# Performance work log

Measured on AMD Instinct MI355X. Metric: run time of the kernel, lower is better.

## Reference

```python
import jax, jax.numpy as jnp
import numpy as np

B, S, F, D, H, L = 32, 512, 40, 512, 8, 4
T = S + 1
DK, DV = D // 2, D          # expand_k=0.5, expand_v=1.0 (fla GLA defaults)
HK, HV = DK // H, DV // H
GLR = 16                    # gate low-rank dim
GLN = 16.0                  # gate logit normalizer
MLP = 4 * D


def sin_pos(t, d, n=10000.0):
    pos = jnp.arange(t, dtype=jnp.float32)[:, None]
    den = jnp.power(n, 2.0 * jnp.arange(d // 2, dtype=jnp.float32) / d)
    e = jnp.zeros((t, d), jnp.float32)
    e = e.at[:, 0::2].set(jnp.sin(pos / den))
    e = e.at[:, 1::2].set(jnp.cos(pos / den))
    return e


def layernorm(x, w, b, eps=1e-5):
    m = x.mean(-1, keepdims=True)
    v = ((x - m) ** 2).mean(-1, keepdims=True)
    return (x - m) * jax.lax.rsqrt(v + eps) * w + b


def bin_norm(x, l1, b1, l2, b2, y1, y2):
    # x: (b, f, s). BiN: temporal z-norm with per-feature affine (X2) +
    # feature z-norm with per-time affine (X1); unbiased std, small std -> 1.
    st = jnp.sqrt(x.var(axis=2, ddof=1, keepdims=True))
    st = jnp.where(st < 1e-4, 1.0, st)
    Z2 = (x - x.mean(axis=2, keepdims=True)) / st
    X2 = l2[None, :, None] * Z2 + b2[None, :, None]
    sf = jnp.sqrt(x.var(axis=1, ddof=1, keepdims=True))
    sf = jnp.where(sf < 1e-4, 1.0, sf)
    Z1 = (x - x.mean(axis=1, keepdims=True)) / sf
    X1 = l1[None, None, :] * Z1 + b1[None, None, :]
    return y1 * X1 + y2 * X2


def gla_attn(x, qw, kw, vw, gw, gkw1, gkw2, gkb2, gnw, ow):
    # Gated linear attention, recurrent form: S_t = exp(gk_t) * S_{t-1} + k_t v_t^T
    b, t, _ = x.shape
    q = (x @ qw).reshape(b, t, H, HK) * (HK ** -0.5)
    k = (x @ kw).reshape(b, t, H, HK)
    v = (x @ vw).reshape(b, t, H, HV)
    g = (x @ gw).reshape(b, t, H, HV)
    gk = (jax.nn.log_sigmoid((x @ gkw1) @ gkw2 + gkb2) / GLN).reshape(b, t, H, HK)

    def step(Sc, inp):
        qt, kt, vt, gt = inp                       # (b,H,HK),(b,H,HK),(b,H,HV),(b,H,HK)
        Sc = Sc * jnp.exp(gt)[..., None] + kt[..., None] * vt[..., None, :]
        return Sc, jnp.einsum('bhk,bhkv->bhv', qt, Sc)

    init = jnp.zeros((b, H, HK, HV), x.dtype)
    to_t = lambda a: jnp.swapaxes(a, 0, 1)        # (t, b, H, dim)
    _, o = jax.lax.scan(step, init, (to_t(q), to_t(k), to_t(v), to_t(gk)))
    o = jnp.swapaxes(o, 0, 1)                     # (b, t, H, HV)
    o = o * jax.lax.rsqrt((o * o).mean(-1, keepdims=True) + 1e-5) * gnw  # head RMSNorm
    o = o * g * jax.nn.sigmoid(g)                 # swish output gate
    return o.reshape(b, t, DV) @ ow


def setup_inputs():
    key = jax.random.key(0)
    ks = iter(jax.random.split(key, 64))
    r = lambda shape, s=0.02: jax.random.normal(next(ks), shape, jnp.float32) * s
    return dict(
        x=jax.random.normal(next(ks), (B, S, F), jnp.float32),
        bin_l1=r((S,), 0.1), bin_b1=jnp.zeros((S,), jnp.float32),
        bin_l2=r((F,), 0.1), bin_b2=jnp.zeros((F,), jnp.float32),
        bin_y1=jnp.float32(0.5), bin_y2=jnp.float32(0.5),
        emb_w=r((F, D)), emb_b=jnp.zeros((D,), jnp.float32),
        cls_token=jnp.zeros((D,), jnp.float32),
        ln1_w=jnp.ones((L, D), jnp.float32), ln1_b=jnp.zeros((L, D), jnp.float32),
        q_w=r((L, D, DK)), k_w=r((L, D, DK)), v_w=r((L, D, DV)), g_w=r((L, D, DV)),
        gk_w1=r((L, D, GLR)), gk_w2=r((L, GLR, DK)), gk_b2=jnp.zeros((L, DK), jnp.float32),
        gnorm_w=jnp.ones((L, HV), jnp.float32),
        o_w=r((L, DV, D)),
        ln2_w=jnp.ones((L, D), jnp.float32), ln2_b=jnp.zeros((L, D), jnp.float32),
        mlp_w1=r((L, D, MLP)), mlp_b1=jnp.zeros((L, MLP), jnp.float32),
        mlp_w2=r((L, MLP, D)), mlp_b2=jnp.zeros((L, D), jnp.float32),
        head_w=r((D, 3)), head_b=jnp.zeros((3,), jnp.float32),
    )


def reference(x, bin_l1, bin_b1, bin_l2, bin_b2, bin_y1, bin_y2, emb_w, emb_b,
              cls_token, ln1_w, ln1_b, q_w, k_w, v_w, g_w, gk_w1, gk_w2, gk_b2,
              gnorm_w, o_w, ln2_w, ln2_b, mlp_w1, mlp_b1, mlp_w2, mlp_b2,
              head_w, head_b):
    h = bin_norm(jnp.swapaxes(x, 1, 2), bin_l1, bin_b1, bin_l2, bin_b2, bin_y1, bin_y2)
    h = jnp.swapaxes(h, 1, 2) @ emb_w + emb_b                    # (b, s, D)
    cls = jnp.broadcast_to(cls_token, (h.shape[0], 1, D))
    h = jnp.concatenate([h, cls], axis=1) + sin_pos(T, D)[None]  # (b, s+1, D)
    for i in range(L):
        a = gla_attn(layernorm(h, ln1_w[i], ln1_b[i]), q_w[i], k_w[i], v_w[i],
                     g_w[i], gk_w1[i], gk_w2[i], gk_b2[i], gnorm_w[i], o_w[i])
        h = h + a
        m = layernorm(h, ln2_w[i], ln2_b[i])
        m = jax.nn.gelu(m @ mlp_w1[i] + mlp_b1[i], approximate=False)
        h = h + m @ mlp_w2[i] + mlp_b2[i]
    return h[:, -1] @ head_w + head_b                            # (b, 3)
```

## Files before the change

### kernel.cpp

```cpp
#include <hip/hip_runtime.h>
#include <hip/hip_bf16.h>
#include <hip/hip_fp16.h>
#include <math.h>

#define Bsz   32
#define Ssz   512
#define Fsz   40
#define Dsz   512
#define Hh    8
#define Lnum  4
#define Tsz   513
#define DKsz  256
#define DVsz  512
#define HKsz  32
#define HVsz  64
#define Msz   (Bsz*Tsz)
#define Mpad  16512
#define MLPsz 2048
#define NCH   16
#define CSZ   33
#define QKVG  1536
#define VOFF  8404992

typedef __attribute__((ext_vector_type(4))) float f32x4;
typedef __attribute__((ext_vector_type(8))) short bf16x8;

__device__ __forceinline__ float bf2f(short s) {
  unsigned int u = ((unsigned int)(unsigned short)s) << 16;
  return __builtin_bit_cast(float, u);
}
__device__ __forceinline__ short f2bf(float f) {
  __hip_bfloat16 b = __float2bfloat16(f);
  return __builtin_bit_cast(short, b);
}

__device__ __forceinline__ float wave_sum(float v) {
#pragma unroll
  for (int off = 32; off > 0; off >>= 1) v += __shfl_xor(v, off, 64);
  return v;
}

__global__ void pos_kernel(float* __restrict__ pos) {
  int idx = blockIdx.x * 256 + threadIdx.x;
  if (idx >= Tsz * Dsz) return;
  int t = idx / Dsz, d = idx % Dsz;
  float e = (float)(2 * (d >> 1)) / (float)Dsz;
  float den = powf(10000.f, e);
  float a = (float)t / den;
  pos[idx] = (d & 1) ? cosf(a) : sinf(a);
}

__global__ void tstat_kernel(const float* __restrict__ x,
                             float* __restrict__ mt, float* __restrict__ rst) {
  int bf = blockIdx.x;
  int b = bf / Fsz, f = bf % Fsz;
  int lane = threadIdx.x;
  const float* xp = x + (size_t)b * Ssz * Fsz + f;
  float s = 0.f, sq = 0.f;
  for (int i = lane; i < Ssz; i += 64) {
    float v = xp[(size_t)i * Fsz];
    s += v; sq += v * v;
  }
  s = wave_sum(s); sq = wave_sum(sq);
  if (lane == 0) {
    float m = s / (float)Ssz;
    float var = (sq - (float)Ssz * m * m) / (float)(Ssz - 1);
    float st = sqrtf(fmaxf(var, 0.f));
    if (st < 1e-4f) st = 1.f;
    mt[bf] = m;
    rst[bf] = 1.f / st;
  }
}

__global__ __launch_bounds__(64) void binorm_kernel(
    const float* __restrict__ x, const float* __restrict__ l1,
    const float* __restrict__ b1, const float* __restrict__ l2,
    const float* __restrict__ b2, const float* __restrict__ y1p,
    const float* __restrict__ y2p, const float* __restrict__ mt,
    const float* __restrict__ rst, float* __restrict__ xbT) {
  int row = blockIdx.x;
  int lane = threadIdx.x;
  int b = row / Tsz, t = row % Tsz;
  bool valid = (row < Msz) && (t < Ssz);
  if (!valid) {
    if (lane < Fsz) xbT[(size_t)lane * Mpad + row] = 0.f;
    return;
  }
  float xv = 0.f;
  const float* xp = x + ((size_t)b * Ssz + t) * Fsz;
  if (lane < Fsz) xv = xp[lane];
  float s  = wave_sum(lane < Fsz ? xv : 0.f);
  float sq = wave_sum(lane < Fsz ? xv * xv : 0.f);
  float m = s / (float)Fsz;
  float var = (sq - (float)Fsz * m * m) / (float)(Fsz - 1);
  float sf = sqrtf(fmaxf(var, 0.f));
  if (sf < 1e-4f) sf = 1.f;
  if (lane < Fsz) {
    float y1 = y1p[0], y2 = y2p[0];
    float z1 = (xv - m) / sf;
    float X1 = l1[t] * z1 + b1[t];
    int bf = b * Fsz + lane;
    float z2 = (xv - mt[bf]) * rst[bf];
    float X2 = l2[lane] * z2 + b2[lane];
    xbT[(size_t)lane * Mpad + row] = y1 * X1 + y2 * X2;
  }
}

__global__ __launch_bounds__(256, 4) void embgemm_kernel(
    const float* __restrict__ xbT, const float* __restrict__ emb_w,
    const float* __restrict__ emb_b, const float* __restrict__ cls,
    const float* __restrict__ pos, float* __restrict__ h) {
  __shared__ float as[Fsz][64];
  __shared__ float bs[Fsz][64];
  int tid = threadIdx.x, tx = tid & 15, ty = tid >> 4;
  int r0 = blockIdx.x * 64, c0 = blockIdx.y * 64;
  for (int idx = tid; idx < Fsz * 64; idx += 256) {
    int f = idx >> 6, r = idx & 63;
    as[f][r] = xbT[(size_t)f * Mpad + r0 + r];
    bs[f][r] = emb_w[f * Dsz + c0 + r];
  }
  __syncthreads();
  float acc[4][4] = {};
#pragma unroll 5
  for (int f = 0; f < Fsz; ++f) {
    float4 a = *(const float4*)&as[f][ty * 4];
    float4 bv = *(const float4*)&bs[f][tx * 4];
    float av[4] = {a.x, a.y, a.z, a.w};
    float bw[4] = {bv.x, bv.y, bv.z, bv.w};
#pragma unroll
    for (int i = 0; i < 4; ++i)
#pragma unroll
      for (int j = 0; j < 4; ++j) acc[i][j] += av[i] * bw[j];
  }
#pragma unroll
  for (int i = 0; i < 4; ++i) {
    int gm = r0 + ty * 4 + i;
    int t = gm % Tsz;
    const float* pp = pos + (size_t)t * Dsz;
    bool iscls = (t == Ssz);
    int gn = c0 + tx * 4;
#pragma unroll
    for (int j = 0; j < 4; ++j) {
      float v = iscls ? (cls[gn + j] + pp[gn + j])
                      : (acc[i][j] + emb_b[gn + j] + pp[gn + j]);
      h[(size_t)gm * Dsz + gn + j] = v;
    }
  }
}

__global__ __launch_bounds__(64) void ln_kernel(
    const float* __restrict__ in, const float* __restrict__ w,
    const float* __restrict__ b, short* __restrict__ out) {
  int row = blockIdx.x, lane = threadIdx.x;
  const float* p = in + (size_t)row * Dsz;
  float4 v0 = *(const float4*)(p + lane * 8);
  float4 v1 = *(const float4*)(p + lane * 8 + 4);
  float s  = v0.x + v0.y + v0.z + v0.w + v1.x + v1.y + v1.z + v1.w;
  float sq = v0.x*v0.x + v0.y*v0.y + v0.z*v0.z + v0.w*v0.w
           + v1.x*v1.x + v1.y*v1.y + v1.z*v1.z + v1.w*v1.w;
  s = wave_sum(s); sq = wave_sum(sq);
  float m = s * (1.f / Dsz);
  float var = sq * (1.f / Dsz) - m * m;
  float r = rsqrtf(var + 1e-5f);
  float4 w0 = *(const float4*)(w + lane * 8);
  float4 w1 = *(const float4*)(w + lane * 8 + 4);
  float4 b0 = *(const float4*)(b + lane * 8);
  float4 b1v = *(const float4*)(b + lane * 8 + 4);
  bf16x8 pk;
  pk[0] = f2bf((v0.x - m) * r * w0.x + b0.x);
  pk[1] = f2bf((v0.y - m) * r * w0.y + b0.y);
  pk[2] = f2bf((v0.z - m) * r * w0.z + b0.z);
  pk[3] = f2bf((v0.w - m) * r * w0.w + b0.w);
  pk[4] = f2bf((v1.x - m) * r * w1.x + b1v.x);
  pk[5] = f2bf((v1.y - m) * r * w1.y + b1v.y);
  pk[6] = f2bf((v1.z - m) * r * w1.z + b1v.z);
  pk[7] = f2bf((v1.w - m) * r * w1.w + b1v.w);
  *(bf16x8*)(out + (size_t)row * Dsz + lane * 8) = pk;
}

__global__ __launch_bounds__(256) void wtall_kernel(
    const float* __restrict__ qw, const float* __restrict__ kw,
    const float* __restrict__ vw, const float* __restrict__ gw,
    const float* __restrict__ ow, const float* __restrict__ m1w,
    const float* __restrict__ m2w, short* __restrict__ qkvT,
    short* __restrict__ owT, short* __restrict__ m1T, short* __restrict__ m2T) {
  __shared__ float t[32][33];
  int bid = blockIdx.x;
  int tx = threadIdx.x & 31, ty = threadIdx.x >> 5;
  const float* W; short* Wt; int K, N, k0, n0, nD;
  if (bid < 768) {
    int kx = bid & 15, ny = bid >> 4;
    int n0g = ny * 32;
    int ld;
    if (n0g < 256)       { W = qw; n0 = n0g;        ld = DKsz; }
    else if (n0g < 512)  { W = kw; n0 = n0g - 256;  ld = DKsz; }
    else if (n0g < 1024) { W = vw; n0 = n0g - 512;  ld = DVsz; }
    else                 { W = gw; n0 = n0g - 1024; ld = DVsz; }
    k0 = kx * 32; K = Dsz; N = ld; Wt = qkvT; nD = n0g;
  } else if (bid < 1024) {
    int idx = bid - 768;
    k0 = (idx & 15) * 32; n0 = (idx >> 4) * 32;
    W = ow; Wt = owT; K = DVsz; N = Dsz; nD = n0;
  } else if (bid < 2048) {
    int idx = bid - 1024;
    k0 = (idx & 15) * 32; n0 = (idx >> 4) * 32;
    W = m1w; Wt = m1T; K = Dsz; N = MLPsz; nD = n0;
  } else {
    int idx = bid - 2048;
    k0 = (idx & 63) * 32; n0 = (idx >> 6) * 32;
    W = m2w; Wt = m2T; K = MLPsz; N = Dsz; nD = n0;
  }
#pragma unroll
  for (int r = 0; r < 32; r += 8)
    t[ty + r][tx] = W[(size_t)(k0 + ty + r) * N + n0 + tx];
  __syncthreads();
#pragma unroll
  for (int r = 0; r < 32; r += 8)
    Wt[(size_t)(nD + ty + r) * K + k0 + tx] = f2bf(t[tx][ty + r]);
}

template<int ACT, int OBF, int SCAT>
__global__ __launch_bounds__(256) void mgemm_kernel(
    const short* __restrict__ A, const short* __restrict__ Bt,
    void* __restrict__ Cv, const float* __restrict__ bias,
    const float* __restrict__ resid, int N, int K) {
  __shared__ short As[128 * 64];
  __shared__ short Bs[128 * 64];
  int tid = threadIdx.x;
  int lane = tid & 63, wid = tid >> 6;
  int wr = wid >> 1, wc = wid & 1;
  int m0 = blockIdx.x * 128, n0 = blockIdx.y * 128;
  f32x4 acc[4][4];
#pragma unroll
  for (int i = 0; i < 4; ++i)
#pragma unroll
    for (int j = 0; j < 4; ++j) acc[i][j] = (f32x4){0.f, 0.f, 0.f, 0.f};

  int kq = lane >> 4;
  int rsel = lane & 15;

  for (int kt = 0; kt < K; kt += 64) {
#pragma unroll
    for (int i = 0; i < 4; ++i) {
      int li = i * 256 + tid;
      int row = li >> 3;
      int gsrc = (li & 7) ^ (row & 7);
      const short* ga = A + (size_t)(m0 + row) * K + kt + gsrc * 8;
      const short* gb = Bt + (size_t)(n0 + row) * K + kt + gsrc * 8;
      int base = (i * 256 + wid * 64) * 8;
      __builtin_amdgcn_global_load_lds(
          (const __attribute__((address_space(1))) unsigned int*)ga,
          (__attribute__((address_space(3))) unsigned int*)&As[base], 16, 0, 0);
      __builtin_amdgcn_global_load_lds(
          (const __attribute__((address_space(1))) unsigned int*)gb,
          (__attribute__((address_space(3))) unsigned int*)&Bs[base], 16, 0, 0);
    }
    __syncthreads();
#pragma unroll
    for (int s = 0; s < 2; ++s) {
      bf16x8 af[4], bfr[4];
#pragma unroll
      for (int i = 0; i < 4; ++i) {
        int row = wr * 64 + i * 16 + rsel;
        int slot = (s * 4 + kq) ^ (row & 7);
        af[i] = *(const bf16x8*)&As[row * 64 + slot * 8];
        int col = wc * 64 + i * 16 + rsel;
        int slotB = (s * 4 + kq) ^ (col & 7);
        bfr[i] = *(const bf16x8*)&Bs[col * 64 + slotB * 8];
      }
#pragma unroll
      for (int i = 0; i < 4; ++i)
#pragma unroll
        for (int j = 0; j < 4; ++j)
          acc[i][j] = __builtin_amdgcn_mfma_f32_16x16x32_bf16(af[i], bfr[j], acc[i][j], 0, 0, 0);
    }
    __syncthreads();
  }

#pragma unroll
  for (int i = 0; i < 4; ++i) {
    int rbase = m0 + wr * 64 + i * 16 + (lane >> 4) * 4;
#pragma unroll
    for (int j = 0; j < 4; ++j) {
      int gn = n0 + wc * 64 + j * 16 + (lane & 15);
      float bv = (SCAT == 0 && bias) ? bias[gn] : 0.f;
#pragma unroll
      for (int r = 0; r < 4; ++r) {
        int gm = rbase + r;
        float v = acc[i][j][r] + bv;
        if (SCAT == 0) {
          if (ACT == 1) v = 0.5f * v * (1.f + erff(v * 0.70710678118654752f));
          if (resid) v += resid[(size_t)gm * N + gn];
          if (OBF) ((short*)Cv)[(size_t)gm * N + gn] = f2bf(v);
          else     ((float*)Cv)[(size_t)gm * N + gn] = v;
        } else {
          if (gm < Msz) {
            int bq = gm / Tsz, tq = gm - bq * Tsz;
            if (gn < 512) {
              int hq = (gn >> 5) & 7;
              int off = (gn & 31) | ((gn & 256) >> 3);
              ((float*)Cv)[(((size_t)bq * 8 + hq) * Tsz + tq) * 64 + off] = v;
            } else if (gn < 1024) {
              int hq = (gn >> 6) & 7;
              ((float*)Cv)[(size_t)VOFF + (((size_t)bq * 8 + hq) * Tsz + tq) * 64 + (gn & 63)] = v;
            } else {
              int hq = (gn >> 6) & 7;
              ((__half*)const_cast<float*>(resid))[(((size_t)bq * 8 + hq) * Tsz + tq) * 64 + (gn & 63)] = __float2half(v);
            }
          }
        }
      }
    }
  }
}

__global__ __launch_bounds__(64) void gk12_kernel(const short* __restrict__ xn,
    const float* __restrict__ w1, const float* __restrict__ w2,
    const float* __restrict__ b2, float* __restrict__ gkeP) {
  int m = blockIdx.x, lane = threadIdx.x;
  __shared__ float xr[512];
  __shared__ float y[16];
  bf16x8 v = *(const bf16x8*)(xn + (size_t)m * Dsz + lane * 8);
#pragma unroll
  for (int e = 0; e < 8; ++e) xr[lane * 8 + e] = bf2f(v[e]);
  __syncthreads();
  int c = lane & 15, q = lane >> 4;
  float acc = 0.f;
#pragma unroll 8
  for (int i = 0; i < 128; ++i) {
    int k = q * 128 + i;
    acc += xr[k] * w1[k * 16 + c];
  }
  acc += __shfl_xor(acc, 16, 64);
  acc += __shfl_xor(acc, 32, 64);
  if (lane < 16) y[c] = acc;
  __syncthreads();
  int b = m / Tsz, t = m - b * Tsz;
#pragma unroll
  for (int p = 0; p < 4; ++p) {
    int n = lane + p * 64;
    float z = b2[n];
#pragma unroll
    for (int r = 0; r < 16; ++r) z += y[r] * w2[r * 256 + n];
    float ls = (z >= 0.f) ? -log1pf(expf(-z)) : z - log1pf(expf(z));
    int hq = n >> 5;
    gkeP[(((size_t)b * 8 + hq) * Tsz + t) * 32 + (n & 31)] = expf(ls * 0.0625f);
  }
}

__global__ __launch_bounds__(64) void scanA_kernel(
    const float* __restrict__ qkP, const float* __restrict__ gkeP,
    float* __restrict__ Ac, float* __restrict__ Bc) {
  int gid = blockIdx.x;
  int bh = gid >> 4, c = gid & 15;
  int lane = threadIdx.x;
  int t0 = c * CSZ;
  int nst = min(CSZ, Tsz - t0);
  __shared__ __align__(16) float s_k[CSZ * 32];
  __shared__ __align__(16) float s_g[CSZ * 32];
  __shared__ __align__(16) float s_v[CSZ * 64];
  const size_t rowbase = (size_t)bh * Tsz + t0;
  const float* qksrc = qkP + rowbase * 64;
  const float* vsrc  = qkP + (size_t)VOFF + rowbase * 64;
  const float* gsrc  = gkeP + rowbase * 32;
  int nkg = nst * 8;
#pragma unroll
  for (int i = 0; i < 5; ++i) {
    int gi = i * 64 + lane;
    if (gi < nkg) {
      int st = gi >> 3, g4 = (gi & 7) * 4;
      __builtin_amdgcn_global_load_lds(
        (const __attribute__((address_space(1))) unsigned int*)(qksrc + (size_t)st * 64 + 32 + g4),
        (__attribute__((address_space(3))) unsigned int*)s_k + i * 256, 16, 0, 0);
      __builtin_amdgcn_global_load_lds(
        (const __attribute__((address_space(1))) unsigned int*)(gsrc + (size_t)gi * 4),
        (__attribute__((address_space(3))) unsigned int*)s_g + i * 256, 16, 0, 0);
    }
  }
  int nv = nst * 16;
#pragma unroll
  for (int i = 0; i < 9; ++i) {
    int gi = i * 64 + lane;
    if (gi < nv)
      __builtin_amdgcn_global_load_lds(
        (const __attribute__((address_space(1))) unsigned int*)(vsrc + (size_t)gi * 4),
        (__attribute__((address_space(3))) unsigned int*)s_v + i * 256, 16, 0, 0);
  }
  float S[32];
#pragma unroll
  for (int i = 0; i < 32; ++i) S[i] = 0.f;
  float ac = 1.f;
  __syncthreads();
  for (int ts = 0; ts < nst; ++ts) {
    float vv = s_v[ts * 64 + lane];
#pragma unroll
    for (int j = 0; j < 8; ++j) {
      float4 kk = *(const float4*)&s_k[ts * 32 + j * 4];
      float4 gg = *(const float4*)&s_g[ts * 32 + j * 4];
      S[4*j+0] = S[4*j+0] * gg.x + kk.x * vv;
      S[4*j+1] = S[4*j+1] * gg.y + kk.y * vv;
      S[4*j+2] = S[4*j+2] * gg.z + kk.z * vv;
      S[4*j+3] = S[4*j+3] * gg.w + kk.w * vv;
    }
    ac *= s_g[ts * 32 + (lane & 31)];
  }
  float* bp = Bc + ((size_t)gid * 64 + lane) * 32;
#pragma unroll
  for (int j = 0; j < 8; ++j)
    *(float4*)(bp + j * 4) = make_float4(S[4*j+0], S[4*j+1], S[4*j+2], S[4*j+3]);
  if (lane < 32) Ac[(size_t)gid * 32 + lane] = ac;
}

__global__ __launch_bounds__(64) void scanB_kernel(
    const float* __restrict__ Ac, float* __restrict__ Bc) {
  int bh = blockIdx.x;
  int lane = threadIdx.x;
  float cur[32];
#pragma unroll
  for (int i = 0; i < 32; ++i) cur[i] = 0.f;
  __shared__ float sA[32];
  for (int c = 0; c < NCH; ++c) {
    size_t gid = (size_t)bh * NCH + c;
    float* bp = Bc + (gid * 64 + lane) * 32;
    __syncthreads();
    if (lane < 32) sA[lane] = Ac[gid * 32 + lane];
    __syncthreads();
    float4 tb[8];
#pragma unroll
    for (int j = 0; j < 8; ++j) tb[j] = *(const float4*)(bp + j * 4);
#pragma unroll
    for (int j = 0; j < 8; ++j)
      *(float4*)(bp + j * 4) = make_float4(cur[4*j+0], cur[4*j+1], cur[4*j+2], cur[4*j+3]);
#pragma unroll
    for (int j = 0; j < 8; ++j) {
      cur[4*j+0] = sA[4*j+0] * cur[4*j+0] + tb[j].x;
      cur[4*j+1] = sA[4*j+1] * cur[4*j+1] + tb[j].y;
      cur[4*j+2] = sA[4*j+2] * cur[4*j+2] + tb[j].z;
      cur[4*j+3] = sA[4*j+3] * cur[4*j+3] + tb[j].w;
    }
  }
}

__global__ __launch_bounds__(64) void scanC_kernel(
    const float* __restrict__ qkP, const __half* __restrict__ gP,
    const float* __restrict__ gkeP, const float* __restrict__ gnw,
    const float* __restrict__ Bc, short* __restrict__ att) {
  int gid = blockIdx.x;
  int bh = gid >> 4, c = gid & 15;
  int b = bh >> 3, hh = bh & 7;
  int lane = threadIdx.x;
  int t0 = c * CSZ;
  int nst = min(CSZ, Tsz - t0);
  __shared__ __align__(16) float s_qk[CSZ * 64];
  __shared__ __align__(16) float s_g[CSZ * 32];
  __shared__ __align__(16) float s_v[CSZ * 64];
  __shared__ __align__(16) __half s_gt[CSZ * 64];
  const size_t rowbase = (size_t)bh * Tsz + t0;
  const float* qksrc = qkP + rowbase * 64;
  const float* vsrc  = qkP + (size_t)VOFF + rowbase * 64;
  const float* gsrc  = gkeP + rowbase * 32;
  const __half* gtsrc = gP + rowbase * 64;
  int n16 = nst * 16;
#pragma unroll
  for (int i = 0; i < 9; ++i) {
    int gi = i * 64 + lane;
    if (gi < n16) {
      __builtin_amdgcn_global_load_lds(
        (const __attribute__((address_space(1))) unsigned int*)(qksrc + (size_t)gi * 4),
        (__attribute__((address_space(3))) unsigned int*)s_qk + i * 256, 16, 0, 0);
      __builtin_amdgcn_global_load_lds(
        (const __attribute__((address_space(1))) unsigned int*)(vsrc + (size_t)gi * 4),
        (__attribute__((address_space(3))) unsigned int*)s_v + i * 256, 16, 0, 0);
    }
  }
  int n8 = nst * 8;
#pragma unroll
  for (int i = 0; i < 5; ++i) {
    int gi = i * 64 + lane;
    if (gi < n8) {
      __builtin_amdgcn_global_load_lds(
        (const __attribute__((address_space(1))) unsigned int*)(gsrc + (size_t)gi * 4),
        (__attribute__((address_space(3))) unsigned int*)s_g + i * 256, 16, 0, 0);
      __builtin_amdgcn_global_load_lds(
        (const __attribute__((address_space(1))) unsigned int*)((const unsigned int*)gtsrc + (size_t)gi * 4),
        (__attribute__((address_space(3))) unsigned int*)s_gt + i * 256, 16, 0, 0);
    }
  }
  float S[32];
  const float* sp = Bc + ((size_t)gid * 64 + lane) * 32;
#pragma unroll
  for (int j = 0; j < 8; ++j) {
    float4 sv4 = *(const float4*)(sp + j * 4);
    S[4*j+0] = sv4.x; S[4*j+1] = sv4.y; S[4*j+2] = sv4.z; S[4*j+3] = sv4.w;
  }
  float gn = gnw[lane];
  __syncthreads();
  for (int ts = 0; ts < nst; ++ts) {
    float vv = s_v[ts * 64 + lane];
    float gv = __half2float(s_gt[ts * 64 + lane]);
    float o = 0.f;
#pragma unroll
    for (int j = 0; j < 8; ++j) {
      float4 qq = *(const float4*)&s_qk[ts * 64 + j * 4];
      float4 kk = *(const float4*)&s_qk[ts * 64 + 32 + j * 4];
      float4 gg = *(const float4*)&s_g[ts * 32 + j * 4];
      S[4*j+0] = S[4*j+0] * gg.x + kk.x * vv;  o += qq.x * S[4*j+0];
      S[4*j+1] = S[4*j+1] * gg.y + kk.y * vv;  o += qq.y * S[4*j+1];
      S[4*j+2] = S[4*j+2] * gg.z + kk.z * vv;  o += qq.z * S[4*j+2];
      S[4*j+3] = S[4*j+3] * gg.w + kk.w * vv;  o += qq.w * S[4*j+3];
    }
    o *= 0.17677669529663689f;
    float ss = wave_sum(o * o);
    float r = rsqrtf(ss * (1.f / 64.f) + 1e-5f);
    float sig = 1.f / (1.f + expf(-gv));
    att[((size_t)b * Tsz + t0 + ts) * DVsz + hh * HVsz + lane] = f2bf(o * r * gn * gv * sig);
  }
}

__global__ __launch_bounds__(64) void head_kernel(
    const float* __restrict__ h, const float* __restrict__ hw,
    const float* __restrict__ hb, float* __restrict__ out) {
  int b = blockIdx.x, lane = threadIdx.x;
  const float* p = h + ((size_t)b * Tsz + Ssz) * Dsz;
  float p0 = 0.f, p1 = 0.f, p2 = 0.f;
#pragma unroll
  for (int j = 0; j < 8; ++j) {
    int d = lane + j * 64;
    float hv = p[d];
    p0 += hv * hw[d * 3 + 0];
    p1 += hv * hw[d * 3 + 1];
    p2 += hv * hw[d * 3 + 2];
  }
  p0 = wave_sum(p0); p1 = wave_sum(p1); p2 = wave_sum(p2);
  if (lane == 0) {
    out[b * 3 + 0] = p0 + hb[0];
    out[b * 3 + 1] = p1 + hb[1];
    out[b * 3 + 2] = p2 + hb[2];
  }
}

extern "C" void kernel_launch(void* const* d_in, const int* in_sizes, int n_in,
                              void* d_out, int out_size, void* d_ws, size_t ws_size,
                              hipStream_t stream) {
  const float* x       = (const float*)d_in[0];
  const float* bin_l1  = (const float*)d_in[1];
  const float* bin_b1  = (const float*)d_in[2];
  const float* bin_l2  = (const float*)d_in[3];
  const float* bin_b2  = (const float*)d_in[4];
  const float* bin_y1  = (const float*)d_in[5];
  const float* bin_y2  = (const float*)d_in[6];
  const float* emb_w   = (const float*)d_in[7];
  const float* emb_b   = (const float*)d_in[8];
  const float* cls     = (const float*)d_in[9];
  const float* ln1_w   = (const float*)d_in[10];
  const float* ln1_b   = (const float*)d_in[11];
  const float* q_w     = (const float*)d_in[12];
  const float* k_w     = (const float*)d_in[13];
  const float* v_w     = (const float*)d_in[14];
  const float* g_w     = (const float*)d_in[15];
  const float* gk_w1   = (const float*)d_in[16];
  const float* gk_w2   = (const float*)d_in[17];
  const float* gk_b2   = (const float*)d_in[18];
  const float* gnorm_w = (const float*)d_in[19];
  const float* o_w     = (const float*)d_in[20];
  const float* ln2_w   = (const float*)d_in[21];
  const float* ln2_b   = (const float*)d_in[22];
  const float* mlp_w1  = (const float*)d_in[23];
  const float* mlp_b1  = (const float*)d_in[24];
  const float* mlp_w2  = (const float*)d_in[25];
  const float* mlp_b2  = (const float*)d_in[26];
  const float* head_w  = (const float*)d_in[27];
  const float* head_b  = (const float*)d_in[28];
  float* out = (float*)d_out;

  char* wptr = (char*)d_ws;
  auto alloc = [&](size_t bytes) { char* p = wptr; wptr += (bytes + 255) & ~(size_t)255; return p; };
  float* pos  = (float*)alloc((size_t)Tsz * Dsz * 4);
  float* h    = (float*)alloc((size_t)Mpad * Dsz * 4);
  short* xn   = (short*)alloc((size_t)Mpad * Dsz * 2);
  float* qkP  = (float*)alloc((size_t)Mpad * MLPsz * 2);
  float* gkeP = (float*)alloc((size_t)256 * Tsz * 32 * 4);
  __half* gP  = (__half*)alloc((size_t)256 * Tsz * 64 * 2);
  float* mt   = (float*)alloc((size_t)Bsz * Fsz * 4);
  float* rst  = (float*)alloc((size_t)Bsz * Fsz * 4);
  float* Ac   = (float*)alloc((size_t)Bsz * Hh * NCH * 32 * 4);
  float* Bc   = (float*)alloc((size_t)Bsz * Hh * NCH * 64 * 32 * 4);
  short* wtr  = (short*)alloc((size_t)3145728 * 2);
  float* xbT  = qkP;
  short* mid  = (short*)qkP;
  short* att  = xn;

  short* qkvT = wtr;
  short* owT  = qkvT + 786432;
  short* m1T  = owT + 262144;
  short* m2T  = m1T + 1048576;

  hipLaunchKernelGGL(pos_kernel, dim3((Tsz * Dsz + 255) / 256), dim3(256), 0, stream, pos);
  hipLaunchKernelGGL(tstat_kernel, dim3(Bsz * Fsz), dim3(64), 0, stream, x, mt, rst);
  hipLaunchKernelGGL(binorm_kernel, dim3(Mpad), dim3(64), 0, stream,
                     x, bin_l1, bin_b1, bin_l2, bin_b2, bin_y1, bin_y2, mt, rst, xbT);
  hipLaunchKernelGGL(embgemm_kernel, dim3(258, 8), dim3(256), 0, stream,
                     xbT, emb_w, emb_b, cls, pos, h);

  dim3 blk256(256);
  for (int l = 0; l < Lnum; ++l) {
    hipLaunchKernelGGL(wtall_kernel, dim3(3072), blk256, 0, stream,
                       q_w + (size_t)l*Dsz*DKsz, k_w + (size_t)l*Dsz*DKsz,
                       v_w + (size_t)l*Dsz*DVsz, g_w + (size_t)l*Dsz*DVsz,
                       o_w + (size_t)l*DVsz*Dsz, mlp_w1 + (size_t)l*Dsz*MLPsz,
                       mlp_w2 + (size_t)l*MLPsz*Dsz, qkvT, owT, m1T, m2T);

    const float* lw1 = ln1_w + l * Dsz;  const float* lb1 = ln1_b + l * Dsz;
    const float* g1w = gk_w1 + (size_t)l * Dsz * 16;
    const float* g2w = gk_w2 + (size_t)l * 16 * DKsz;
    const float* g2b = gk_b2 + (size_t)l * DKsz;
    const float* gnw = gnorm_w + l * HVsz;
    const float* lw2 = ln2_w + l * Dsz;  const float* lb2 = ln2_b + l * Dsz;
    const float* m1b = mlp_b1 + (size_t)l * MLPsz;
    const float* m2b = mlp_b2 + (size_t)l * Dsz;

    hipLaunchKernelGGL(ln_kernel, dim3(Msz), dim3(64), 0, stream, h, lw1, lb1, xn);

    hipLaunchKernelGGL((mgemm_kernel<0,0,1>), dim3(129, 12), blk256, 0, stream,
                       xn, qkvT, (void*)qkP, (const float*)nullptr, (const float*)gP, QKVG, Dsz);
    hipLaunchKernelGGL(gk12_kernel, dim3(Msz), dim3(64), 0, stream, xn, g1w, g2w, g2b, gkeP);

    hipLaunchKernelGGL(scanA_kernel, dim3(Bsz * Hh * NCH), dim3(64), 0, stream,
                       qkP, gkeP, Ac, Bc);
    hipLaunchKernelGGL(scanB_kernel, dim3(Bsz * Hh), dim3(64), 0, stream, Ac, Bc);
    hipLaunchKernelGGL(scanC_kernel, dim3(Bsz * Hh * NCH), dim3(64), 0, stream,
                       qkP, gP, gkeP, gnw, Bc, att);

    hipLaunchKernelGGL((mgemm_kernel<0,0,0>), dim3(129, 4), blk256, 0, stream,
                       att, owT, (void*)h, (const float*)nullptr, h, Dsz, DVsz);

    hipLaunchKernelGGL(ln_kernel, dim3(Msz), dim3(64), 0, stream, h, lw2, lb2, xn);
    hipLaunchKernelGGL((mgemm_kernel<1,1,0>), dim3(129, 16), blk256, 0, stream,
                       xn, m1T, (void*)mid, m1b, (const float*)nullptr, MLPsz, Dsz);
    hipLaunchKernelGGL((mgemm_kernel<0,0,0>), dim3(129, 4), blk256, 0, stream,
                       mid, m2T, (void*)h, m2b, h, Dsz, MLPsz);
  }

  hipLaunchKernelGGL(head_kernel, dim3(Bsz), dim3(64), 0, stream, h, head_w, head_b, out);
}
```

Baseline: 1.760 ms.

## Double-buffer LDS in bf16 GEMM to overlap global loads with MFMA

Adds a second LDS buffer for both A and B tiles in the MFMA GEMM kernel. The next K-tile is prefetched with global_load_lds while the current tile is computed, using a partial vmcnt wait and raw barriers in place of __syncthreads. MFMA sections also raise wave priority with s_setprio. This targets exposed global-load latency in the GEMMs. In exchange it doubles LDS use to 64KB per block, which may lower occupancy, and it relies on a hand-counted vmcnt value being correct.

```diff
diff --git a/kernel.cpp b/kernel.cpp
--- a/kernel.cpp
+++ b/kernel.cpp
@@ -224,8 +224,8 @@
     const short* __restrict__ A, const short* __restrict__ Bt,
     void* __restrict__ Cv, const float* __restrict__ bias,
     const float* __restrict__ resid, int N, int K) {
-  __shared__ short As[128 * 64];
-  __shared__ short Bs[128 * 64];
+  __shared__ short As[2][128 * 64];
+  __shared__ short Bs[2][128 * 64];
   int tid = threadIdx.x;
   int lane = tid & 63, wid = tid >> 6;
   int wr = wid >> 1, wc = wid & 1;
@@ -239,7 +239,7 @@
   int kq = lane >> 4;
   int rsel = lane & 15;
 
-  for (int kt = 0; kt < K; kt += 64) {
+  auto stage = [&](int kt, int bsel) {
 #pragma unroll
     for (int i = 0; i < 4; ++i) {
       int li = i * 256 + tid;
@@ -250,12 +250,14 @@
       int base = (i * 256 + wid * 64) * 8;
       __builtin_amdgcn_global_load_lds(
           (const __attribute__((address_space(1))) unsigned int*)ga,
-          (__attribute__((address_space(3))) unsigned int*)&As[base], 16, 0, 0);
+          (__attribute__((address_space(3))) unsigned int*)&As[bsel][base], 16, 0, 0);
       __builtin_amdgcn_global_load_lds(
           (const __attribute__((address_space(1))) unsigned int*)gb,
-          (__attribute__((address_space(3))) unsigned int*)&Bs[base], 16, 0, 0);
-    }
-    __syncthreads();
+          (__attribute__((address_space(3))) unsigned int*)&Bs[bsel][base], 16, 0, 0);
+    }
+  };
+
+  auto compute = [&](int bsel) {
 #pragma unroll
     for (int s = 0; s < 2; ++s) {
       bf16x8 af[4], bfr[4];
@@ -263,19 +265,38 @@
       for (int i = 0; i < 4; ++i) {
         int row = wr * 64 + i * 16 + rsel;
         int slot = (s * 4 + kq) ^ (row & 7);
-        af[i] = *(const bf16x8*)&As[row * 64 + slot * 8];
+        af[i] = *(const bf16x8*)&As[bsel][row * 64 + slot * 8];
         int col = wc * 64 + i * 16 + rsel;
         int slotB = (s * 4 + kq) ^ (col & 7);
-        bfr[i] = *(const bf16x8*)&Bs[col * 64 + slotB * 8];
+        bfr[i] = *(const bf16x8*)&Bs[bsel][col * 64 + slotB * 8];
       }
+      __builtin_amdgcn_s_setprio(1);
 #pragma unroll
       for (int i = 0; i < 4; ++i)
 #pragma unroll
         for (int j = 0; j < 4; ++j)
           acc[i][j] = __builtin_amdgcn_mfma_f32_16x16x32_bf16(af[i], bfr[j], acc[i][j], 0, 0, 0);
-    }
-    __syncthreads();
-  }
+      __builtin_amdgcn_s_setprio(0);
+    }
+  };
+
+  int nt = K >> 6;
+  stage(0, 0);
+  int cur = 0;
+  for (int t = 0; t < nt - 1; ++t) {
+    stage((t + 1) << 6, cur ^ 1);
+    asm volatile("s_waitcnt vmcnt(8)" ::: "memory");
+    __builtin_amdgcn_s_barrier();
+    asm volatile("" ::: "memory");
+    compute(cur);
+    __builtin_amdgcn_s_barrier();
+    asm volatile("" ::: "memory");
+    cur ^= 1;
+  }
+  asm volatile("s_waitcnt vmcnt(0)" ::: "memory");
+  __builtin_amdgcn_s_barrier();
+  asm volatile("" ::: "memory");
+  compute(cur);
 
 #pragma unroll
   for (int i = 0; i < 4; ++i) {
```

After: 2.125 ms. 20.8% more time.
